# Optimization experiments

Hardware: AMD Instinct MI355X
Metric: run time of the kernel (lower is better)

## Reference

```python
import jax, jax.numpy as jnp
import numpy as np

N_ATOMS = 200_000
N_EDGES = 4_000_000

# physical / numerical constants closed over by BambooBase
ELE_FACTOR = 332.0637  # Coulomb constant, kcal*A/mol/e^2
EWALD_F = 1.12837917   # 2/sqrt(pi)
EWALD_P = 0.3275911
EWALD_A = (0.254829592, -0.284496736, 1.421413741, -1.453152027, 1.061405429)
COUL_BETA = 18.7
COUL_R0 = 2.2
DISP_CUTOFF = 10.0
G_EWALD = 0.3          # typical Ewald splitting parameter (1/A)


def setup_inputs() -> dict:
    key = jax.random.key(0)
    k1, k2, k3, k4, k5, k6, k7 = jax.random.split(key, 7)
    row = jax.random.randint(k1, (N_EDGES,), 0, N_ATOMS, dtype=jnp.int32)
    col = jax.random.randint(k2, (N_EDGES,), 0, N_ATOMS, dtype=jnp.int32)
    # edge displacement vectors: random direction, radius in [1, 10) Angstrom
    direction = jax.random.normal(k3, (N_EDGES, 3), dtype=jnp.float32)
    direction = direction / jnp.linalg.norm(direction, axis=-1, keepdims=True)
    radius = jax.random.uniform(k4, (N_EDGES, 1), minval=1.0, maxval=10.0, dtype=jnp.float32)
    dij = direction * radius
    charge = 0.3 * jax.random.normal(k5, (N_ATOMS,), dtype=jnp.float32)
    c6 = jax.random.uniform(k6, (N_ATOMS,), minval=1.0, maxval=100.0, dtype=jnp.float32)
    r0 = jax.random.uniform(k7, (N_ATOMS,), minval=2.0, maxval=4.0, dtype=jnp.float32)
    return {"row": row, "col": col, "dij": dij, "charge": charge, "c6": c6, "r0": r0}


def reference(row, col, dij, charge, c6, r0):
    # ---- shared per-edge distance ----
    rij = jnp.sqrt(jnp.sum(dij * dij, axis=-1))  # [E]

    # ---- get_coulomb ----
    prefactor = ELE_FACTOR * charge[row] * charge[col] / rij
    damp = jax.nn.sigmoid(COUL_BETA / COUL_R0 * (rij - COUL_R0))
    # torch.nn.Softplus(beta=b)(x) == softplus(b*x)/b
    sp = jax.nn.softplus(COUL_BETA * (rij - COUL_R0) / COUL_R0) / COUL_BETA
    s = rij / COUL_R0 / (1.0 + sp)
    ecoul = prefactor * s
    fcoul = prefactor * damp * s * s
    # Ewald short-range correction (erfc via Horner polynomial)
    grij = G_EWALD * rij
    expm2 = jnp.exp(-grij * grij)
    t = 1.0 / (1.0 + EWALD_P * grij)
    a0, a1, a2, a3, a4 = EWALD_A
    erfc = t * (a0 + t * (a1 + t * (a2 + t * (a3 + t * a4)))) * expm2
    ecoul = ecoul + prefactor * (erfc - 1.0)
    fcoul = fcoul + prefactor * (erfc + EWALD_F * grij * expm2 - 1.0)
    coul_fij = dij * (fcoul / (rij * rij))[:, None]

    # ---- get_dispersion (D3-CSO) ----
    c6ij = jnp.sqrt(c6[row] * c6[col])
    r0ij = 0.5 * (r0[row] + r0[col])
    r6 = rij ** 6 + 4.5 ** 6
    e = jnp.exp(rij - 2.5 * r0ij)
    cso = 0.85 + 0.82 / (1.0 + e)
    edisp = -c6ij / r6 * cso
    fdisp = -6.0 * c6ij * rij ** 5 / (r6 * r6) * cso - c6ij / r6 * (0.82 * e / (1.0 + e) ** 2)
    disp_fij = dij * (fdisp / rij)[:, None]
    edisp = edisp + c6ij / DISP_CUTOFF ** 6

    return ecoul, coul_fij, edisp, disp_fij
```

## Files before the change

### kernel.cpp

```cpp
#include <hip/hip_runtime.h>
#include <math.h>

#define C_ELE   332.0637f
#define C_EWF   1.12837917f
#define C_EWP   0.3275911f
#define C_A0    0.254829592f
#define C_A1   -0.284496736f
#define C_A2    1.421413741f
#define C_A3   -1.453152027f
#define C_A4    1.061405429f
#define C_BETA  18.7f
#define C_R0    2.2f
#define C_GEW   0.3f
#define C_45P6  8303.765625f
#define C_DC6I  1e-6f

typedef float vf4 __attribute__((ext_vector_type(4)));
typedef int   vi4 __attribute__((ext_vector_type(4)));

__device__ __forceinline__ float frcp(float x) { return __builtin_amdgcn_rcpf(x); }

struct EdgeOut { float ec, fx, fy, fz, ed, gx, gy, gz; };

__device__ __forceinline__ EdgeOut edge_compute(
    vf4 ar, vf4 ac, float dx, float dy, float dz)
{
    float r2   = dx * dx + dy * dy + dz * dz;
    float rij  = sqrtf(r2);
    float rinv = frcp(rij);

    float pref = C_ELE * ar.x * ac.x * rinv;
    float x    = (C_BETA / C_R0) * (rij - C_R0);
    float ax   = fabsf(x);
    float ex   = __expf(-ax);
    float den  = frcp(1.0f + ex);
    float damp = (x >= 0.0f) ? den : ex * den;
    float sp   = (fmaxf(x, 0.0f) + __logf(1.0f + ex)) * (1.0f / C_BETA);
    float s    = rij * (1.0f / C_R0) * frcp(1.0f + sp);

    float grij  = C_GEW * rij;
    float expm2 = __expf(-grij * grij);
    float t     = frcp(1.0f + C_EWP * grij);
    float erfc  = t * (C_A0 + t * (C_A1 + t * (C_A2 + t * (C_A3 + t * C_A4)))) * expm2;

    EdgeOut o;
    o.ec = pref * (s + erfc - 1.0f);
    float fcl = pref * (damp * s * s + erfc + C_EWF * grij * expm2 - 1.0f);
    float fsc = fcl * frcp(r2);
    o.fx = dx * fsc; o.fy = dy * fsc; o.fz = dz * fsc;

    float c6ij  = sqrtf(ar.y * ac.y);
    float r0ij  = 0.5f * (ar.z + ac.z);
    float r6    = r2 * r2 * r2 + C_45P6;
    float r6i   = frcp(r6);
    float e     = __expf(rij - 2.5f * r0ij);
    float onep  = frcp(1.0f + e);
    float cso   = 0.85f + 0.82f * onep;
    o.ed = -c6ij * r6i * cso + c6ij * C_DC6I;
    float r5  = r2 * r2 * rij;
    float fd  = -6.0f * c6ij * r5 * r6i * r6i * cso - c6ij * r6i * (0.82f * e * onep * onep);
    float gsc = fd * rinv;
    o.gx = dx * gsc; o.gy = dy * gsc; o.gz = dz * gsc;
    return o;
}

__global__ __launch_bounds__(256) void pack_atoms(
    const float* __restrict__ charge, const float* __restrict__ c6a,
    const float* __restrict__ r0a, vf4* __restrict__ tbl, int N)
{
    int i = blockIdx.x * blockDim.x + threadIdx.x;
    if (i < N) {
        vf4 v = { charge[i], c6a[i], r0a[i], 0.0f };
        tbl[i] = v;
    }
}

__global__ __launch_bounds__(256) void bamboo_vec4(
    const int* __restrict__ row, const int* __restrict__ col,
    const float* __restrict__ dij,
    const vf4* __restrict__ tbl,
    float* __restrict__ out, int E)
{
    int g    = blockIdx.x * blockDim.x + threadIdx.x;
    int base = g * 4;
    if (base >= E) return;

    float* __restrict__ ec_o = out;
    float* __restrict__ cf_o = out + (size_t)E;
    float* __restrict__ ed_o = out + (size_t)4 * E;
    float* __restrict__ df_o = out + (size_t)5 * E;

    vi4 rr = __builtin_nontemporal_load((const vi4*)(row + base));
    vi4 cc = __builtin_nontemporal_load((const vi4*)(col + base));
    const float* dp = dij + (size_t)base * 3;
    vf4 d0 = __builtin_nontemporal_load((const vf4*)(dp + 0));
    vf4 d1 = __builtin_nontemporal_load((const vf4*)(dp + 4));
    vf4 d2 = __builtin_nontemporal_load((const vf4*)(dp + 8));
    __builtin_amdgcn_sched_barrier(0);

    vf4 a0r = tbl[rr.x]; vf4 a0c = tbl[cc.x];
    vf4 a1r = tbl[rr.y]; vf4 a1c = tbl[cc.y];
    vf4 a2r = tbl[rr.z]; vf4 a2c = tbl[cc.z];
    vf4 a3r = tbl[rr.w]; vf4 a3c = tbl[cc.w];
    __builtin_amdgcn_sched_barrier(0);

    EdgeOut o0 = edge_compute(a0r, a0c, d0.x, d0.y, d0.z);
    EdgeOut o1 = edge_compute(a1r, a1c, d0.w, d1.x, d1.y);
    EdgeOut o2 = edge_compute(a2r, a2c, d1.z, d1.w, d2.x);
    EdgeOut o3 = edge_compute(a3r, a3c, d2.y, d2.z, d2.w);

    vf4 ec4 = { o0.ec, o1.ec, o2.ec, o3.ec };
    vf4 ed4 = { o0.ed, o1.ed, o2.ed, o3.ed };
    __builtin_nontemporal_store(ec4, (vf4*)(ec_o + base));
    __builtin_nontemporal_store(ed4, (vf4*)(ed_o + base));

    vf4 f0 = { o0.fx, o0.fy, o0.fz, o1.fx };
    vf4 f1 = { o1.fy, o1.fz, o2.fx, o2.fy };
    vf4 f2 = { o2.fz, o3.fx, o3.fy, o3.fz };
    float* cfp = cf_o + (size_t)base * 3;
    __builtin_nontemporal_store(f0, (vf4*)(cfp + 0));
    __builtin_nontemporal_store(f1, (vf4*)(cfp + 4));
    __builtin_nontemporal_store(f2, (vf4*)(cfp + 8));

    vf4 g0 = { o0.gx, o0.gy, o0.gz, o1.gx };
    vf4 g1 = { o1.gy, o1.gz, o2.gx, o2.gy };
    vf4 g2 = { o2.gz, o3.gx, o3.gy, o3.gz };
    float* dfp = df_o + (size_t)base * 3;
    __builtin_nontemporal_store(g0, (vf4*)(dfp + 0));
    __builtin_nontemporal_store(g1, (vf4*)(dfp + 4));
    __builtin_nontemporal_store(g2, (vf4*)(dfp + 8));
}

__global__ __launch_bounds__(256) void bamboo_scalar(
    const int* __restrict__ row, const int* __restrict__ col,
    const float* __restrict__ dij,
    const float* __restrict__ charge, const float* __restrict__ c6a,
    const float* __restrict__ r0a,
    float* __restrict__ out, int E, int start)
{
    int j = start + blockIdx.x * blockDim.x + threadIdx.x;
    if (j >= E) return;
    float* ec_o = out;
    float* cf_o = out + (size_t)E;
    float* ed_o = out + (size_t)4 * E;
    float* df_o = out + (size_t)5 * E;
    int r = row[j], c = col[j];
    vf4 ar = { charge[r], c6a[r], r0a[r], 0.0f };
    vf4 ac = { charge[c], c6a[c], r0a[c], 0.0f };
    EdgeOut o = edge_compute(ar, ac,
                             dij[3 * (size_t)j], dij[3 * (size_t)j + 1], dij[3 * (size_t)j + 2]);
    ec_o[j] = o.ec; ed_o[j] = o.ed;
    cf_o[3 * (size_t)j] = o.fx; cf_o[3 * (size_t)j + 1] = o.fy; cf_o[3 * (size_t)j + 2] = o.fz;
    df_o[3 * (size_t)j] = o.gx; df_o[3 * (size_t)j + 1] = o.gy; df_o[3 * (size_t)j + 2] = o.gz;
}

extern "C" void kernel_launch(void* const* d_in, const int* in_sizes, int n_in,
                              void* d_out, int out_size, void* d_ws, size_t ws_size,
                              hipStream_t stream) {
    const int*   row    = (const int*)d_in[0];
    const int*   col    = (const int*)d_in[1];
    const float* dij    = (const float*)d_in[2];
    const float* charge = (const float*)d_in[3];
    const float* c6a    = (const float*)d_in[4];
    const float* r0a    = (const float*)d_in[5];
    float* out = (float*)d_out;
    int E = in_sizes[0];
    int N = in_sizes[3];

    size_t need = (size_t)N * sizeof(vf4);
    if (ws_size >= need && ((uintptr_t)d_ws % 16) == 0 && (E & 3) == 0) {
        vf4* tbl = (vf4*)d_ws;
        pack_atoms<<<(N + 255) / 256, 256, 0, stream>>>(charge, c6a, r0a, tbl, N);
        int groups = E / 4;
        bamboo_vec4<<<(groups + 255) / 256, 256, 0, stream>>>(row, col, dij, tbl, out, E);
    } else {
        bamboo_scalar<<<(E + 255) / 256, 256, 0, stream>>>(row, col, dij, charge, c6a, r0a, out, E, 0);
    }
}
```

Measured before the change: 233.3 us.

## Software-pipeline edge kernel with persistent grid-stride loop and double buffering

Replaces the one-shot vec4 kernel with a persistent grid-stride kernel capped at 768 blocks that double-buffers index, displacement and atom-table gathers. Loads for the next two iterations are issued before computing the current group, so gather latency overlaps with math. This trades occupancy, through launch_bounds(256,3) and extra live registers, for explicit prefetch, and relies on the compiler keeping the ping-pong arrays in registers.

```diff
diff --git a/kernel.cpp b/kernel.cpp
--- a/kernel.cpp
+++ b/kernel.cpp
@@ -75,60 +75,100 @@
     }
 }
 
-__global__ __launch_bounds__(256) void bamboo_vec4(
+
+#define PHASE(CUR, NXT, IR_CUR, IC_CUR, IR_NXT, IC_NXT, DCUR, DNXT)            \
+  {                                                                            \
+    if (g >= G) return;                                                        \
+    int gn1 = g + s;                                                           \
+    int gn2 = gn1 + s;                                                         \
+    bool v1 = gn1 < G, v2 = gn2 < G;                                           \
+    if (v2) {                                                                  \
+      IR_NXT = __builtin_nontemporal_load((const vi4*)(row + 4 * (size_t)gn2));\
+      IC_NXT = __builtin_nontemporal_load((const vi4*)(col + 4 * (size_t)gn2));\
+    }                                                                          \
+    if (v1) {                                                                  \
+      const float* dp_ = dij + (size_t)gn1 * 12;                               \
+      DNXT[0] = __builtin_nontemporal_load((const vf4*)(dp_ + 0));             \
+      DNXT[1] = __builtin_nontemporal_load((const vf4*)(dp_ + 4));             \
+      DNXT[2] = __builtin_nontemporal_load((const vf4*)(dp_ + 8));             \
+      NXT[0] = tbl[IR_CUR.x]; NXT[1] = tbl[IC_CUR.x];                          \
+      NXT[2] = tbl[IR_CUR.y]; NXT[3] = tbl[IC_CUR.y];                          \
+      NXT[4] = tbl[IR_CUR.z]; NXT[5] = tbl[IC_CUR.z];                          \
+      NXT[6] = tbl[IR_CUR.w]; NXT[7] = tbl[IC_CUR.w];                          \
+    }                                                                          \
+    __builtin_amdgcn_sched_barrier(0);                                         \
+    {                                                                          \
+      EdgeOut o0 = edge_compute(CUR[0], CUR[1], DCUR[0].x, DCUR[0].y, DCUR[0].z); \
+      EdgeOut o1 = edge_compute(CUR[2], CUR[3], DCUR[0].w, DCUR[1].x, DCUR[1].y); \
+      EdgeOut o2 = edge_compute(CUR[4], CUR[5], DCUR[1].z, DCUR[1].w, DCUR[2].x); \
+      EdgeOut o3 = edge_compute(CUR[6], CUR[7], DCUR[2].y, DCUR[2].z, DCUR[2].w); \
+      int base = g * 4;                                                        \
+      vf4 ec4 = { o0.ec, o1.ec, o2.ec, o3.ec };                                \
+      vf4 ed4 = { o0.ed, o1.ed, o2.ed, o3.ed };                                \
+      __builtin_nontemporal_store(ec4, (vf4*)(ec_o + base));                   \
+      __builtin_nontemporal_store(ed4, (vf4*)(ed_o + base));                   \
+      vf4 f0v = { o0.fx, o0.fy, o0.fz, o1.fx };                                \
+      vf4 f1v = { o1.fy, o1.fz, o2.fx, o2.fy };                                \
+      vf4 f2v = { o2.fz, o3.fx, o3.fy, o3.fz };                                \
+      float* cfp = cf_o + (size_t)base * 3;                                    \
+      __builtin_nontemporal_store(f0v, (vf4*)(cfp + 0));                       \
+      __builtin_nontemporal_store(f1v, (vf4*)(cfp + 4));                       \
+      __builtin_nontemporal_store(f2v, (vf4*)(cfp + 8));                       \
+      vf4 g0v = { o0.gx, o0.gy, o0.gz, o1.gx };                                \
+      vf4 g1v = { o1.gy, o1.gz, o2.gx, o2.gy };                                \
+      vf4 g2v = { o2.gz, o3.gx, o3.gy, o3.gz };                                \
+      float* dfp = df_o + (size_t)base * 3;                                    \
+      __builtin_nontemporal_store(g0v, (vf4*)(dfp + 0));                       \
+      __builtin_nontemporal_store(g1v, (vf4*)(dfp + 4));                       \
+      __builtin_nontemporal_store(g2v, (vf4*)(dfp + 8));                       \
+    }                                                                          \
+    g = gn1;                                                                   \
+  }
+
+__global__ __launch_bounds__(256, 3) void bamboo_pipe(
     const int* __restrict__ row, const int* __restrict__ col,
     const float* __restrict__ dij,
     const vf4* __restrict__ tbl,
     float* __restrict__ out, int E)
 {
-    int g    = blockIdx.x * blockDim.x + threadIdx.x;
-    int base = g * 4;
-    if (base >= E) return;
+    const int G = E >> 2;
+    const int s = gridDim.x * blockDim.x;
+    int g = blockIdx.x * blockDim.x + threadIdx.x;
+    if (g >= G) return;
 
     float* __restrict__ ec_o = out;
     float* __restrict__ cf_o = out + (size_t)E;
     float* __restrict__ ed_o = out + (size_t)4 * E;
     float* __restrict__ df_o = out + (size_t)5 * E;
 
-    vi4 rr = __builtin_nontemporal_load((const vi4*)(row + base));
-    vi4 cc = __builtin_nontemporal_load((const vi4*)(col + base));
-    const float* dp = dij + (size_t)base * 3;
-    vf4 d0 = __builtin_nontemporal_load((const vf4*)(dp + 0));
-    vf4 d1 = __builtin_nontemporal_load((const vf4*)(dp + 4));
-    vf4 d2 = __builtin_nontemporal_load((const vf4*)(dp + 8));
-    __builtin_amdgcn_sched_barrier(0);
-
-    vf4 a0r = tbl[rr.x]; vf4 a0c = tbl[cc.x];
-    vf4 a1r = tbl[rr.y]; vf4 a1c = tbl[cc.y];
-    vf4 a2r = tbl[rr.z]; vf4 a2c = tbl[cc.z];
-    vf4 a3r = tbl[rr.w]; vf4 a3c = tbl[cc.w];
-    __builtin_amdgcn_sched_barrier(0);
-
-    EdgeOut o0 = edge_compute(a0r, a0c, d0.x, d0.y, d0.z);
-    EdgeOut o1 = edge_compute(a1r, a1c, d0.w, d1.x, d1.y);
-    EdgeOut o2 = edge_compute(a2r, a2c, d1.z, d1.w, d2.x);
-    EdgeOut o3 = edge_compute(a3r, a3c, d2.y, d2.z, d2.w);
-
-    vf4 ec4 = { o0.ec, o1.ec, o2.ec, o3.ec };
-    vf4 ed4 = { o0.ed, o1.ed, o2.ed, o3.ed };
-    __builtin_nontemporal_store(ec4, (vf4*)(ec_o + base));
-    __builtin_nontemporal_store(ed4, (vf4*)(ed_o + base));
-
-    vf4 f0 = { o0.fx, o0.fy, o0.fz, o1.fx };
-    vf4 f1 = { o1.fy, o1.fz, o2.fx, o2.fy };
-    vf4 f2 = { o2.fz, o3.fx, o3.fy, o3.fz };
-    float* cfp = cf_o + (size_t)base * 3;
-    __builtin_nontemporal_store(f0, (vf4*)(cfp + 0));
-    __builtin_nontemporal_store(f1, (vf4*)(cfp + 4));
-    __builtin_nontemporal_store(f2, (vf4*)(cfp + 8));
-
-    vf4 g0 = { o0.gx, o0.gy, o0.gz, o1.gx };
-    vf4 g1 = { o1.gy, o1.gz, o2.gx, o2.gy };
-    vf4 g2 = { o2.gz, o3.gx, o3.gy, o3.gz };
-    float* dfp = df_o + (size_t)base * 3;
-    __builtin_nontemporal_store(g0, (vf4*)(dfp + 0));
-    __builtin_nontemporal_store(g1, (vf4*)(dfp + 4));
-    __builtin_nontemporal_store(g2, (vf4*)(dfp + 8));
+    vf4 A[8], B[8];
+    vf4 D0[3], D1[3];
+    vi4 rI0, cI0, rI1, cI1;
+
+    {
+        vi4 rr = __builtin_nontemporal_load((const vi4*)(row + 4 * (size_t)g));
+        vi4 cc = __builtin_nontemporal_load((const vi4*)(col + 4 * (size_t)g));
+        const float* dp = dij + (size_t)g * 12;
+        D0[0] = __builtin_nontemporal_load((const vf4*)(dp + 0));
+        D0[1] = __builtin_nontemporal_load((const vf4*)(dp + 4));
+        D0[2] = __builtin_nontemporal_load((const vf4*)(dp + 8));
+        int g1 = g + s;
+        if (g1 < G) {
+            rI0 = __builtin_nontemporal_load((const vi4*)(row + 4 * (size_t)g1));
+            cI0 = __builtin_nontemporal_load((const vi4*)(col + 4 * (size_t)g1));
+        }
+        __builtin_amdgcn_sched_barrier(0);
+        A[0] = tbl[rr.x]; A[1] = tbl[cc.x];
+        A[2] = tbl[rr.y]; A[3] = tbl[cc.y];
+        A[4] = tbl[rr.z]; A[5] = tbl[cc.z];
+        A[6] = tbl[rr.w]; A[7] = tbl[cc.w];
+        __builtin_amdgcn_sched_barrier(0);
+    }
+
+    for (;;) {
+        PHASE(A, B, rI0, cI0, rI1, cI1, D0, D1);
+        PHASE(B, A, rI1, cI1, rI0, cI0, D1, D0);
+    }
 }
 
 __global__ __launch_bounds__(256) void bamboo_scalar(
@@ -172,7 +212,9 @@
         vf4* tbl = (vf4*)d_ws;
         pack_atoms<<<(N + 255) / 256, 256, 0, stream>>>(charge, c6a, r0a, tbl, N);
         int groups = E / 4;
-        bamboo_vec4<<<(groups + 255) / 256, 256, 0, stream>>>(row, col, dij, tbl, out, E);
+        int blocks = (groups + 255) / 256;
+        if (blocks > 768) blocks = 768;
+        bamboo_pipe<<<blocks, 256, 0, stream>>>(row, col, dij, tbl, out, E);
     } else {
         bamboo_scalar<<<(E + 255) / 256, 256, 0, stream>>>(row, col, dij, charge, c6a, r0a, out, E, 0);
     }
```

Result: slower. 239.1 us (+2.5%).

## Stage edge vectors and force outputs through LDS for coalesced global access

Applied to the files above, without the earlier changes.

Loads the 3-component displacement vectors per 1024-edge tile as lane-contiguous vf4 chunks, transposes them through shared memory, and likewise stages coulomb and dispersion force outputs in shared memory before writing contiguous vf4 stores. This targets the strided 48-byte-per-lane access pattern of the previous kernel. It adds two block barriers and about 40KB of LDS per block, which may reduce occupancy, and handles the non-multiple-of-1024 tail with a scalar launch.

```diff
diff --git a/kernel.cpp b/kernel.cpp
--- a/kernel.cpp
+++ b/kernel.cpp
@@ -75,27 +75,32 @@
     }
 }
 
-__global__ __launch_bounds__(256) void bamboo_vec4(
+__global__ __launch_bounds__(256) void bamboo_lds(
     const int* __restrict__ row, const int* __restrict__ col,
     const float* __restrict__ dij,
     const vf4* __restrict__ tbl,
     float* __restrict__ out, int E)
 {
-    int g    = blockIdx.x * blockDim.x + threadIdx.x;
-    int base = g * 4;
-    if (base >= E) return;
+    __shared__ float s_dij[256 * 13];
+    __shared__ float s_cf [256 * 13];
+    __shared__ float s_df [256 * 13];
+
+    const int t     = threadIdx.x;
+    const int ebase = blockIdx.x << 10;
+    const int gbase = ebase + t * 4;
 
     float* __restrict__ ec_o = out;
     float* __restrict__ cf_o = out + (size_t)E;
     float* __restrict__ ed_o = out + (size_t)4 * E;
     float* __restrict__ df_o = out + (size_t)5 * E;
 
-    vi4 rr = __builtin_nontemporal_load((const vi4*)(row + base));
-    vi4 cc = __builtin_nontemporal_load((const vi4*)(col + base));
-    const float* dp = dij + (size_t)base * 3;
-    vf4 d0 = __builtin_nontemporal_load((const vf4*)(dp + 0));
-    vf4 d1 = __builtin_nontemporal_load((const vf4*)(dp + 4));
-    vf4 d2 = __builtin_nontemporal_load((const vf4*)(dp + 8));
+    vi4 rr = __builtin_nontemporal_load((const vi4*)(row + gbase));
+    vi4 cc = __builtin_nontemporal_load((const vi4*)(col + gbase));
+
+    const vf4* dstream = (const vf4*)(dij + (size_t)ebase * 3);
+    vf4 d0 = __builtin_nontemporal_load(dstream + (0 * 256 + t));
+    vf4 d1 = __builtin_nontemporal_load(dstream + (1 * 256 + t));
+    vf4 d2 = __builtin_nontemporal_load(dstream + (2 * 256 + t));
     __builtin_amdgcn_sched_barrier(0);
 
     vf4 a0r = tbl[rr.x]; vf4 a0c = tbl[cc.x];
@@ -104,31 +109,56 @@
     vf4 a3r = tbl[rr.w]; vf4 a3c = tbl[cc.w];
     __builtin_amdgcn_sched_barrier(0);
 
-    EdgeOut o0 = edge_compute(a0r, a0c, d0.x, d0.y, d0.z);
-    EdgeOut o1 = edge_compute(a1r, a1c, d0.w, d1.x, d1.y);
-    EdgeOut o2 = edge_compute(a2r, a2c, d1.z, d1.w, d2.x);
-    EdgeOut o3 = edge_compute(a3r, a3c, d2.y, d2.z, d2.w);
+    {
+        int v, q, r, b;
+        v = 0 * 256 + t; q = v / 3; r = v - 3 * q; b = q * 13 + 4 * r;
+        s_dij[b + 0] = d0.x; s_dij[b + 1] = d0.y; s_dij[b + 2] = d0.z; s_dij[b + 3] = d0.w;
+        v = 1 * 256 + t; q = v / 3; r = v - 3 * q; b = q * 13 + 4 * r;
+        s_dij[b + 0] = d1.x; s_dij[b + 1] = d1.y; s_dij[b + 2] = d1.z; s_dij[b + 3] = d1.w;
+        v = 2 * 256 + t; q = v / 3; r = v - 3 * q; b = q * 13 + 4 * r;
+        s_dij[b + 0] = d2.x; s_dij[b + 1] = d2.y; s_dij[b + 2] = d2.z; s_dij[b + 3] = d2.w;
+    }
+    __syncthreads();
+
+    float d[12];
+    #pragma unroll
+    for (int m = 0; m < 12; ++m) d[m] = s_dij[t * 13 + m];
+
+    EdgeOut o0 = edge_compute(a0r, a0c, d[0],  d[1],  d[2]);
+    EdgeOut o1 = edge_compute(a1r, a1c, d[3],  d[4],  d[5]);
+    EdgeOut o2 = edge_compute(a2r, a2c, d[6],  d[7],  d[8]);
+    EdgeOut o3 = edge_compute(a3r, a3c, d[9],  d[10], d[11]);
 
     vf4 ec4 = { o0.ec, o1.ec, o2.ec, o3.ec };
     vf4 ed4 = { o0.ed, o1.ed, o2.ed, o3.ed };
-    __builtin_nontemporal_store(ec4, (vf4*)(ec_o + base));
-    __builtin_nontemporal_store(ed4, (vf4*)(ed_o + base));
-
-    vf4 f0 = { o0.fx, o0.fy, o0.fz, o1.fx };
-    vf4 f1 = { o1.fy, o1.fz, o2.fx, o2.fy };
-    vf4 f2 = { o2.fz, o3.fx, o3.fy, o3.fz };
-    float* cfp = cf_o + (size_t)base * 3;
-    __builtin_nontemporal_store(f0, (vf4*)(cfp + 0));
-    __builtin_nontemporal_store(f1, (vf4*)(cfp + 4));
-    __builtin_nontemporal_store(f2, (vf4*)(cfp + 8));
-
-    vf4 g0 = { o0.gx, o0.gy, o0.gz, o1.gx };
-    vf4 g1 = { o1.gy, o1.gz, o2.gx, o2.gy };
-    vf4 g2 = { o2.gz, o3.gx, o3.gy, o3.gz };
-    float* dfp = df_o + (size_t)base * 3;
-    __builtin_nontemporal_store(g0, (vf4*)(dfp + 0));
-    __builtin_nontemporal_store(g1, (vf4*)(dfp + 4));
-    __builtin_nontemporal_store(g2, (vf4*)(dfp + 8));
+    __builtin_nontemporal_store(ec4, (vf4*)(ec_o + gbase));
+    __builtin_nontemporal_store(ed4, (vf4*)(ed_o + gbase));
+
+    {
+        float* cf = s_cf + t * 13;
+        float* df = s_df + t * 13;
+        cf[0]  = o0.fx; cf[1]  = o0.fy; cf[2]  = o0.fz;
+        cf[3]  = o1.fx; cf[4]  = o1.fy; cf[5]  = o1.fz;
+        cf[6]  = o2.fx; cf[7]  = o2.fy; cf[8]  = o2.fz;
+        cf[9]  = o3.fx; cf[10] = o3.fy; cf[11] = o3.fz;
+        df[0]  = o0.gx; df[1]  = o0.gy; df[2]  = o0.gz;
+        df[3]  = o1.gx; df[4]  = o1.gy; df[5]  = o1.gz;
+        df[6]  = o2.gx; df[7]  = o2.gy; df[8]  = o2.gz;
+        df[9]  = o3.gx; df[10] = o3.gy; df[11] = o3.gz;
+    }
+    __syncthreads();
+
+    vf4* cf_out = (vf4*)(cf_o + (size_t)ebase * 3);
+    vf4* df_out = (vf4*)(df_o + (size_t)ebase * 3);
+    #pragma unroll
+    for (int j = 0; j < 3; ++j) {
+        int v = j * 256 + t;
+        int q = v / 3, r = v - 3 * q, b = q * 13 + 4 * r;
+        vf4 wc = { s_cf[b], s_cf[b + 1], s_cf[b + 2], s_cf[b + 3] };
+        __builtin_nontemporal_store(wc, cf_out + v);
+        vf4 wd = { s_df[b], s_df[b + 1], s_df[b + 2], s_df[b + 3] };
+        __builtin_nontemporal_store(wd, df_out + v);
+    }
 }
 
 __global__ __launch_bounds__(256) void bamboo_scalar(
@@ -168,11 +198,16 @@
     int N = in_sizes[3];
 
     size_t need = (size_t)N * sizeof(vf4);
-    if (ws_size >= need && ((uintptr_t)d_ws % 16) == 0 && (E & 3) == 0) {
+    if (ws_size >= need && ((uintptr_t)d_ws % 16) == 0) {
         vf4* tbl = (vf4*)d_ws;
         pack_atoms<<<(N + 255) / 256, 256, 0, stream>>>(charge, c6a, r0a, tbl, N);
-        int groups = E / 4;
-        bamboo_vec4<<<(groups + 255) / 256, 256, 0, stream>>>(row, col, dij, tbl, out, E);
+        int ntiles = E >> 10;
+        int tail   = ntiles << 10;
+        if (ntiles > 0)
+            bamboo_lds<<<ntiles, 256, 0, stream>>>(row, col, dij, tbl, out, E);
+        if (tail < E)
+            bamboo_scalar<<<(E - tail + 255) / 256, 256, 0, stream>>>(
+                row, col, dij, charge, c6a, r0a, out, E, tail);
     } else {
         bamboo_scalar<<<(E + 255) / 256, 256, 0, stream>>>(row, col, dij, charge, c6a, r0a, out, E, 0);
     }
```

Result: no change. 231.2 us (-0.9%).
